# Optimization experiments

Measured on AMD Instinct MI355X. Metric: run time of the kernel, lower is better.

## Reference

```python
import jax, jax.numpy as jnp
import numpy as np

B, S, NX, NH = 4, 1024, 1024, 16
HD = NX // NH  # 64


def setup_inputs() -> dict:
    key = jax.random.key(0)
    k1, k2, k3 = jax.random.split(key, 3)
    return {
        "hidden_states": jax.random.normal(k1, (B, S, NX), dtype=jnp.float32),
        "c_attn_w": jax.random.normal(k2, (NX, 3 * NX), dtype=jnp.float32) * 0.02,
        "c_attn_b": jnp.zeros((3 * NX,), dtype=jnp.float32),
        "c_proj_w": jax.random.normal(k3, (NX, NX), dtype=jnp.float32) * 0.02,
        "c_proj_b": jnp.zeros((NX,), dtype=jnp.float32),
    }


def reference(hidden_states, c_attn_w, c_attn_b, c_proj_w, c_proj_b):
    # Conv1D fused QKV projection: x @ W + b, then split into q,k,v
    qkv = hidden_states @ c_attn_w + c_attn_b  # [B,S,3*NX]
    q, k, v = jnp.split(qkv, 3, axis=-1)
    # split heads -> [B, H, S, D]
    def heads(x):
        return x.reshape(B, S, NH, HD).transpose(0, 2, 1, 3)
    q, k, v = heads(q), heads(k), heads(v)
    # scores: q @ k^T / sqrt(D)  (scale=True; NOTE: no causal mask in this fork)
    w = jnp.einsum("bhqd,bhkd->bhqk", q, k) / jnp.sqrt(jnp.asarray(HD, q.dtype))
    w = jax.nn.softmax(w, axis=-1)
    a = jnp.einsum("bhqk,bhkd->bhqd", w, v)  # [B,H,S,D]
    # merge heads -> [B,S,NX]
    a = a.transpose(0, 2, 1, 3).reshape(B, S, NX)
    # output projection (dropout is identity in eval)
    return a @ c_proj_w + c_proj_b
```

## Files before the change

kernel.cpp:

```cpp
#include <hip/hip_runtime.h>
#include <hip/hip_fp16.h>
#include <cmath>

constexpr int Bb  = 4;
constexpr int Ss  = 1024;
constexpr int NXc = 1024;
constexpr int NHc = 16;
constexpr int HDc = 64;

typedef __bf16    bf16x8 __attribute__((ext_vector_type(8)));
typedef _Float16  f16x8  __attribute__((ext_vector_type(8)));
typedef float     f32x4  __attribute__((ext_vector_type(4)));
typedef unsigned short ushortT;
typedef ushortT ushort8v __attribute__((ext_vector_type(8)));

#define QSCALE 0.18033688011112042f

__device__ __forceinline__ ushortT f2h_bits(float x) {
  return __half_as_ushort(__float2half(x));
}

__device__ __forceinline__ void gll16(const void* g, void* l) {
  __builtin_amdgcn_global_load_lds(
      (const __attribute__((address_space(1))) unsigned int*)g,
      (__attribute__((address_space(3))) unsigned int*)l, 16, 0, 0);
}

__device__ __forceinline__ void drain_vmem() {
  asm volatile("s_waitcnt vmcnt(0)" ::: "memory");
  __builtin_amdgcn_sched_barrier(0);
}

__global__ __launch_bounds__(256) void prep_all(
    const float* __restrict__ hs, const float* __restrict__ aw,
    const float* __restrict__ pw,
    ushortT* __restrict__ hF, ushortT* __restrict__ awT,
    ushortT* __restrict__ pwT)
{
  const int bid = blockIdx.x;
  if (bid < 4096) {
    int i = (bid * 256 + threadIdx.x) * 4;
    float4 v = *reinterpret_cast<const float4*>(&hs[i]);
    *reinterpret_cast<ushort4*>(&hF[i]) =
        make_ushort4(f2h_bits(v.x), f2h_bits(v.y), f2h_bits(v.z), f2h_bits(v.w));
    return;
  }
  __shared__ float tile[32][33];
  const int tx = threadIdx.x & 31, ty = threadIdx.x >> 5;
  if (bid < 7168) {
    const int b2 = bid - 4096;
    const int n0 = (b2 % 96) * 32, k0 = (b2 / 96) * 32;
    #pragma unroll
    for (int i = 0; i < 4; ++i)
      tile[ty + i * 8][tx] = aw[(size_t)(k0 + ty + i * 8) * 3072 + n0 + tx];
    __syncthreads();
    #pragma unroll
    for (int i = 0; i < 4; ++i)
      awT[(size_t)(n0 + ty + i * 8) * 1024 + k0 + tx] = f2h_bits(tile[tx][ty + i * 8]);
  } else {
    const int b2 = bid - 7168;
    const int n0 = (b2 & 31) * 32, k0 = (b2 >> 5) * 32;
    #pragma unroll
    for (int i = 0; i < 4; ++i)
      tile[ty + i * 8][tx] = pw[(size_t)(k0 + ty + i * 8) * 1024 + n0 + tx];
    __syncthreads();
    #pragma unroll
    for (int i = 0; i < 4; ++i)
      pwT[(size_t)(n0 + ty + i * 8) * 1024 + k0 + tx] = f2h_bits(tile[tx][ty + i * 8]);
  }
}

__global__ __launch_bounds__(256) void gemm_f16_qkv(
    const ushortT* __restrict__ A16, const ushortT* __restrict__ B16,
    const float* __restrict__ bias,
    ushortT* __restrict__ Qb, ushortT* __restrict__ Kb,
    ushortT* __restrict__ Vt, int M, int N, int K)
{
  constexpr int BK = 64;
  __shared__ ushortT smem[32768];

  const int t    = threadIdx.x;
  const int lane = t & 63;
  const int w    = t >> 6;
  const int wr   = w >> 1, wc = w & 1;
  const int lin = blockIdx.y * 24 + blockIdx.x;
  const int swz = (lin & 7) * 96 + (lin >> 3);
  const int m0 = (swz / 24) * 128;
  const int n0 = (swz % 24) * 128;
  const int l15 = lane & 15;
  const int g   = lane >> 4;

  const int srow  = w * 32 + (lane >> 3);
  const int sslot = (lane & 7) ^ (lane >> 3);

  f32x4 acc[4][4];
  #pragma unroll
  for (int m = 0; m < 4; ++m)
    #pragma unroll
    for (int n = 0; n < 4; ++n)
      #pragma unroll
      for (int r = 0; r < 4; ++r) acc[m][n][r] = 0.f;

  const ushortT* pA = A16 + (size_t)(m0 + srow) * K + sslot * 8;
  const ushortT* pB = B16 + (size_t)(n0 + srow) * K + sslot * 8;

  auto STAGE = [&](ushortT* buf, int k0) {
    #pragma unroll
    for (int i = 0; i < 4; ++i) {
      const size_t gstep = (size_t)i * 8 * K + k0;
      const int    loff  = (w * 32 + i * 8) * BK;
      gll16(pA + gstep, &buf[loff]);
      gll16(pB + gstep, &buf[8192 + loff]);
    }
  };

  const int arow = wr * 64 + l15;
  const int bcol = wc * 64 + l15;

  auto COMPUTE = [&](const ushortT* buf) {
    const ushortT* sA = buf;
    const ushortT* sB = buf + 8192;
    #pragma unroll
    for (int c = 0; c < 2; ++c) {
      const int slot = c * 4 + g;
      f16x8 af[4], bf[4];
      #pragma unroll
      for (int m = 0; m < 4; ++m) {
        int r   = arow + m * 16;
        int off = r * BK + ((slot ^ (r & 7)) * 8);
        af[m] = *reinterpret_cast<const f16x8*>(&sA[off]);
      }
      #pragma unroll
      for (int n = 0; n < 4; ++n) {
        int r   = bcol + n * 16;
        int off = r * BK + ((slot ^ (r & 7)) * 8);
        bf[n] = *reinterpret_cast<const f16x8*>(&sB[off]);
      }
      #pragma unroll
      for (int m = 0; m < 4; ++m)
        #pragma unroll
        for (int n = 0; n < 4; ++n)
          acc[m][n] = __builtin_amdgcn_mfma_f32_16x16x32_f16(af[m], bf[n], acc[m][n], 0, 0, 0);
    }
  };

  const int nt = K / BK;
  STAGE(&smem[0], 0);
  drain_vmem();
  __syncthreads();
  for (int tt = 0; tt < nt; tt += 2) {
    if (tt + 1 < nt) STAGE(&smem[16384], (tt + 1) * BK);
    COMPUTE(&smem[0]);
    drain_vmem();
    __syncthreads();
    if (tt + 2 < nt) STAGE(&smem[0], (tt + 2) * BK);
    COMPUTE(&smem[16384]);
    drain_vmem();
    __syncthreads();
  }

  const int region = n0 >> 10;
  if (region < 2) {
    #pragma unroll
    for (int n = 0; n < 4; ++n) {
      int col_g = n0 + wc * 64 + n * 16 + l15;
      int colm  = col_g & 1023;
      float bv  = bias[col_g];
      #pragma unroll
      for (int m = 0; m < 4; ++m) {
        int row = m0 + wr * 64 + m * 16 + (g << 2);
        #pragma unroll
        for (int r = 0; r < 4; ++r) {
          float v = acc[m][n][r] + bv;
          if (region == 0)
            Qb[(size_t)(row + r) * 1024 + colm] = f2h_bits(v * QSCALE);
          else
            Kb[(size_t)(row + r) * 1024 + colm] = f2h_bits(v);
        }
      }
    }
  } else {
    ushortT* T = smem;
    #pragma unroll
    for (int n = 0; n < 4; ++n) {
      int cl   = wc * 64 + n * 16 + l15;
      float bv = bias[n0 + cl];
      #pragma unroll
      for (int m = 0; m < 4; ++m) {
        int rl = wr * 64 + m * 16 + (g << 2);
        #pragma unroll
        for (int r = 0; r < 4; ++r)
          T[cl * 136 + rl + r] = f2h_bits(acc[m][n][r] + bv);
      }
    }
    __syncthreads();
    const int c  = t >> 1;
    const int rh = (t & 1) * 64;
    const int nn = (n0 - 2048) + c;
    const int hh = nn >> 6, dd = nn & 63;
    const int bb = m0 >> 10;
    const int sl = (m0 & 1023) + rh;
    size_t vbase = ((size_t)((bb * 16 + hh) * 64 + dd)) * 1024 + sl;
    #pragma unroll
    for (int j = 0; j < 8; ++j) {
      ushort8v v = *reinterpret_cast<const ushort8v*>(&T[c * 136 + rh + j * 8]);
      *reinterpret_cast<ushort8v*>(&Vt[vbase + j * 8]) = v;
    }
  }
}

__global__ __launch_bounds__(256) void gemm_f16s(
    const ushortT* __restrict__ A16, const ushortT* __restrict__ B16,
    const float* __restrict__ bias, float* __restrict__ C,
    int M, int N, int K)
{
  constexpr int BK = 64;
  __shared__ ushortT smem[32768];

  const int t    = threadIdx.x;
  const int lane = t & 63;
  const int w    = t >> 6;
  const int wr   = w >> 1, wc = w & 1;
  const int lin = blockIdx.y * 8 + blockIdx.x;
  const int swz = (lin & 7) * 32 + (lin >> 3);
  const int m0 = (swz / 8) * 128;
  const int n0 = (swz % 8) * 128;
  const int l15 = lane & 15;
  const int g   = lane >> 4;

  const int srow  = w * 32 + (lane >> 3);
  const int sslot = (lane & 7) ^ (lane >> 3);

  f32x4 acc[4][4];
  #pragma unroll
  for (int m = 0; m < 4; ++m)
    #pragma unroll
    for (int n = 0; n < 4; ++n)
      #pragma unroll
      for (int r = 0; r < 4; ++r) acc[m][n][r] = 0.f;

  const ushortT* pA = A16 + (size_t)(m0 + srow) * K + sslot * 8;
  const ushortT* pB = B16 + (size_t)(n0 + srow) * K + sslot * 8;

  auto STAGE = [&](ushortT* buf, int k0) {
    #pragma unroll
    for (int i = 0; i < 4; ++i) {
      const size_t gstep = (size_t)i * 8 * K + k0;
      const int    loff  = (w * 32 + i * 8) * BK;
      gll16(pA + gstep, &buf[loff]);
      gll16(pB + gstep, &buf[8192 + loff]);
    }
  };

  const int arow = wr * 64 + l15;
  const int bcol = wc * 64 + l15;

  auto COMPUTE = [&](const ushortT* buf) {
    const ushortT* sA = buf;
    const ushortT* sB = buf + 8192;
    #pragma unroll
    for (int c = 0; c < 2; ++c) {
      const int slot = c * 4 + g;
      f16x8 af[4], bf[4];
      #pragma unroll
      for (int m = 0; m < 4; ++m) {
        int r   = arow + m * 16;
        int off = r * BK + ((slot ^ (r & 7)) * 8);
        af[m] = *reinterpret_cast<const f16x8*>(&sA[off]);
      }
      #pragma unroll
      for (int n = 0; n < 4; ++n) {
        int r   = bcol + n * 16;
        int off = r * BK + ((slot ^ (r & 7)) * 8);
        bf[n] = *reinterpret_cast<const f16x8*>(&sB[off]);
      }
      #pragma unroll
      for (int m = 0; m < 4; ++m)
        #pragma unroll
        for (int n = 0; n < 4; ++n)
          acc[m][n] = __builtin_amdgcn_mfma_f32_16x16x32_f16(af[m], bf[n], acc[m][n], 0, 0, 0);
    }
  };

  const int nt = K / BK;
  STAGE(&smem[0], 0);
  drain_vmem();
  __syncthreads();
  for (int tt = 0; tt < nt; tt += 2) {
    if (tt + 1 < nt) STAGE(&smem[16384], (tt + 1) * BK);
    COMPUTE(&smem[0]);
    drain_vmem();
    __syncthreads();
    if (tt + 2 < nt) STAGE(&smem[0], (tt + 2) * BK);
    COMPUTE(&smem[16384]);
    drain_vmem();
    __syncthreads();
  }

  #pragma unroll
  for (int n = 0; n < 4; ++n) {
    int col  = n0 + wc * 64 + n * 16 + l15;
    float bv = bias[col];
    #pragma unroll
    for (int m = 0; m < 4; ++m) {
      int row = m0 + wr * 64 + m * 16 + (g << 2);
      #pragma unroll
      for (int r = 0; r < 4; ++r)
        C[(size_t)(row + r) * N + col] = acc[m][n][r] + bv;
    }
  }
}

__global__ __launch_bounds__(256) void attn_mfma(
    const ushortT* __restrict__ Qb, const ushortT* __restrict__ Kb,
    const ushortT* __restrict__ Vt, ushortT* __restrict__ xF)
{
  __shared__ ushortT sK[64 * 64];
  __shared__ ushortT sV[64 * 64];
  __shared__ ushortT sP[64 * 64];

  const int t    = threadIdx.x;
  const int lane = t & 63;
  const int w    = t >> 6;
  const int bh = blockIdx.x, b = bh >> 4, h = bh & 15;
  const int q0 = blockIdx.y * 64;
  const int l15 = lane & 15;
  const int g   = lane >> 4;

  f16x8 qa[2];
  #pragma unroll
  for (int ks = 0; ks < 2; ++ks) {
    size_t addr = (size_t)(b * 1024 + q0 + w * 16 + l15) * 1024
                  + h * 64 + ks * 32 + g * 8;
    qa[ks] = *reinterpret_cast<const f16x8*>(&Qb[addr]);
  }

  f16x8 ones;
  #pragma unroll
  for (int j = 0; j < 8; ++j) ones[j] = (_Float16)1.0f;

  const int srow  = lane >> 3;
  const int sslot = (lane & 7) ^ srow;

  f32x4 O[4];
  f32x4 lO;
  #pragma unroll
  for (int r = 0; r < 4; ++r) lO[r] = 0.f;
  #pragma unroll
  for (int n = 0; n < 4; ++n)
    #pragma unroll
    for (int r = 0; r < 4; ++r) O[n][r] = 0.f;

  for (int kt = 0; kt < 16; ++kt) {
    const int k0 = kt * 64;
    #pragma unroll
    for (int i = 0; i < 2; ++i) {
      int r = w * 16 + i * 8 + srow;
      gll16(&Kb[(size_t)(b * 1024 + k0 + r) * 1024 + h * 64 + sslot * 8],
            &sK[(w * 16 + i * 8) * 64]);
      gll16(&Vt[((size_t)bh * 64 + r) * 1024 + k0 + sslot * 8],
            &sV[(w * 16 + i * 8) * 64]);
    }
    __syncthreads();

    f32x4 sc[4];
    #pragma unroll
    for (int n = 0; n < 4; ++n)
      #pragma unroll
      for (int r = 0; r < 4; ++r) sc[n][r] = 0.f;

    __builtin_amdgcn_s_setprio(1);
    #pragma unroll
    for (int ks = 0; ks < 2; ++ks) {
      f16x8 kb[4];
      #pragma unroll
      for (int n = 0; n < 4; ++n) {
        int row = n * 16 + l15;
        kb[n] = *reinterpret_cast<const f16x8*>(
            &sK[row * 64 + (((g + ks * 4) ^ (row & 7)) * 8)]);
      }
      #pragma unroll
      for (int n = 0; n < 4; ++n)
        sc[n] = __builtin_amdgcn_mfma_f32_16x16x32_f16(qa[ks], kb[n], sc[n], 0, 0, 0);
    }
    __builtin_amdgcn_s_setprio(0);

    #pragma unroll
    for (int n = 0; n < 4; ++n)
      #pragma unroll
      for (int r = 0; r < 4; ++r)
        sc[n][r] = exp2f(sc[n][r]);

    #pragma unroll
    for (int n = 0; n < 4; ++n)
      #pragma unroll
      for (int r = 0; r < 4; ++r) {
        int prow = w * 16 + g * 4 + r;
        int c    = n * 16 + l15;
        int off2 = prow * 64 + ((((c >> 3) ^ (prow & 7)) << 3) | (c & 7));
        sP[off2] = f2h_bits(sc[n][r]);
      }

    __builtin_amdgcn_s_setprio(1);
    #pragma unroll
    for (int ks = 0; ks < 2; ++ks) {
      f16x8 vb[4], pa;
      #pragma unroll
      for (int n = 0; n < 4; ++n) {
        int rd = n * 16 + l15;
        vb[n] = *reinterpret_cast<const f16x8*>(
            &sV[rd * 64 + (((g + ks * 4) ^ (rd & 7)) * 8)]);
      }
      {
        int pr = w * 16 + l15;
        pa = *reinterpret_cast<const f16x8*>(
            &sP[pr * 64 + (((g + ks * 4) ^ (pr & 7)) * 8)]);
      }
      #pragma unroll
      for (int n = 0; n < 4; ++n)
        O[n] = __builtin_amdgcn_mfma_f32_16x16x32_f16(pa, vb[n], O[n], 0, 0, 0);
      lO = __builtin_amdgcn_mfma_f32_16x16x32_f16(pa, ones, lO, 0, 0, 0);
    }
    __builtin_amdgcn_s_setprio(0);
    __syncthreads();
  }

  #pragma unroll
  for (int r = 0; r < 4; ++r) {
    float inv = 1.f / lO[r];
    #pragma unroll
    for (int n = 0; n < 4; ++n) {
      size_t off = (size_t)(b * 1024 + q0 + w * 16 + g * 4 + r) * 1024
                   + h * 64 + n * 16 + l15;
      xF[off] = f2h_bits(O[n][r] * inv);
    }
  }
}

extern "C" void kernel_launch(void* const* d_in, const int* in_sizes, int n_in,
                              void* d_out, int out_size, void* d_ws, size_t ws_size,
                              hipStream_t stream) {
  const float* hs = (const float*)d_in[0];
  const float* aw = (const float*)d_in[1];
  const float* ab = (const float*)d_in[2];
  const float* pw = (const float*)d_in[3];
  const float* pb = (const float*)d_in[4];
  float* out = (float*)d_out;

  char* ws = (char*)d_ws;
  const int M = Bb * Ss;

  ushortT* hF  = (ushortT*)(ws);
  ushortT* awT = (ushortT*)(ws + ( 8u << 20));
  ushortT* pwT = (ushortT*)(ws + (14u << 20));
  ushortT* Qb  = (ushortT*)(ws + (18u << 20));
  ushortT* Kb  = (ushortT*)(ws + (26u << 20));
  ushortT* Vt  = (ushortT*)(ws + (34u << 20));
  ushortT* xF  = (ushortT*)(ws + (42u << 20));

  dim3 blk(256);

  prep_all<<<8192, blk, 0, stream>>>(hs, aw, pw, hF, awT, pwT);
  gemm_f16_qkv<<<dim3(24, 32), blk, 0, stream>>>(
      hF, awT, ab, Qb, Kb, Vt, M, 3 * NXc, NXc);
  attn_mfma<<<dim3(Bb * NHc, Ss / 64), blk, 0, stream>>>(Qb, Kb, Vt, xF);
  gemm_f16s<<<dim3(8, 32), blk, 0, stream>>>(
      xF, pwT, pb, out, M, NXc, NXc);
}
```

Before: 100.3 us.

## Split attention KV range across two blocks and combine partials in new kernel

Result: slower. 105.0 us (+4.7%).

```diff
diff --git a/kernel.cpp b/kernel.cpp
--- a/kernel.cpp
+++ b/kernel.cpp
@@ -18,6 +18,9 @@
 
 __device__ __forceinline__ ushortT f2h_bits(float x) {
   return __half_as_ushort(__float2half(x));
+}
+__device__ __forceinline__ float h2f(ushortT h) {
+  return __half2float(__ushort_as_half(h));
 }
 
 __device__ __forceinline__ void gll16(const void* g, void* l) {
@@ -313,7 +316,8 @@
 
 __global__ __launch_bounds__(256) void attn_mfma(
     const ushortT* __restrict__ Qb, const ushortT* __restrict__ Kb,
-    const ushortT* __restrict__ Vt, ushortT* __restrict__ xF)
+    const ushortT* __restrict__ Vt,
+    ushortT* __restrict__ Op, float* __restrict__ lP)
 {
   __shared__ ushortT sK[64 * 64];
   __shared__ ushortT sV[64 * 64];
@@ -324,6 +328,7 @@
   const int w    = t >> 6;
   const int bh = blockIdx.x, b = bh >> 4, h = bh & 15;
   const int q0 = blockIdx.y * 64;
+  const int half = blockIdx.z;
   const int l15 = lane & 15;
   const int g   = lane >> 4;
 
@@ -351,7 +356,7 @@
     #pragma unroll
     for (int r = 0; r < 4; ++r) O[n][r] = 0.f;
 
-  for (int kt = 0; kt < 16; ++kt) {
+  for (int kt = half * 8; kt < half * 8 + 8; ++kt) {
     const int k0 = kt * 64;
     #pragma unroll
     for (int i = 0; i < 2; ++i) {
@@ -369,7 +374,6 @@
       #pragma unroll
       for (int r = 0; r < 4; ++r) sc[n][r] = 0.f;
 
-    __builtin_amdgcn_s_setprio(1);
     #pragma unroll
     for (int ks = 0; ks < 2; ++ks) {
       f16x8 kb[4];
@@ -383,7 +387,6 @@
       for (int n = 0; n < 4; ++n)
         sc[n] = __builtin_amdgcn_mfma_f32_16x16x32_f16(qa[ks], kb[n], sc[n], 0, 0, 0);
     }
-    __builtin_amdgcn_s_setprio(0);
 
     #pragma unroll
     for (int n = 0; n < 4; ++n)
@@ -401,7 +404,6 @@
         sP[off2] = f2h_bits(sc[n][r]);
       }
 
-    __builtin_amdgcn_s_setprio(1);
     #pragma unroll
     for (int ks = 0; ks < 2; ++ks) {
       f16x8 vb[4], pa;
@@ -421,20 +423,42 @@
         O[n] = __builtin_amdgcn_mfma_f32_16x16x32_f16(pa, vb[n], O[n], 0, 0, 0);
       lO = __builtin_amdgcn_mfma_f32_16x16x32_f16(pa, ones, lO, 0, 0, 0);
     }
-    __builtin_amdgcn_s_setprio(0);
-    __syncthreads();
-  }
-
+    __syncthreads();
+  }
+
+  const size_t obase = (size_t)half * (4096ull * 1024ull);
   #pragma unroll
   for (int r = 0; r < 4; ++r) {
-    float inv = 1.f / lO[r];
+    int qrow = q0 + w * 16 + g * 4 + r;
+    if (l15 == 0)
+      lP[half * 65536 + (b * 16 + h) * 1024 + qrow] = lO[r];
     #pragma unroll
     for (int n = 0; n < 4; ++n) {
-      size_t off = (size_t)(b * 1024 + q0 + w * 16 + g * 4 + r) * 1024
-                   + h * 64 + n * 16 + l15;
-      xF[off] = f2h_bits(O[n][r] * inv);
-    }
-  }
+      size_t off = obase + (size_t)(b * 1024 + qrow) * 1024 + h * 64 + n * 16 + l15;
+      Op[off] = f2h_bits(O[n][r]);
+    }
+  }
+}
+
+__global__ __launch_bounds__(256) void combine_kernel(
+    const ushortT* __restrict__ Op, const float* __restrict__ lP,
+    ushortT* __restrict__ xF)
+{
+  int i = (blockIdx.x * 256 + threadIdx.x) * 8;
+  int row = i >> 10;
+  int col = i & 1023;
+  int b = row >> 10;
+  int q = row & 1023;
+  int h = col >> 6;
+  int lidx = (b * 16 + h) * 1024 + q;
+  float inv = 1.f / (lP[lidx] + lP[65536 + lidx]);
+  ushort8v o1 = *reinterpret_cast<const ushort8v*>(&Op[i]);
+  ushort8v o2 = *reinterpret_cast<const ushort8v*>(&Op[4194304 + i]);
+  ushort8v o;
+  #pragma unroll
+  for (int j = 0; j < 8; ++j)
+    o[j] = f2h_bits((h2f(o1[j]) + h2f(o2[j])) * inv);
+  *reinterpret_cast<ushort8v*>(&xF[i]) = o;
 }
 
 extern "C" void kernel_launch(void* const* d_in, const int* in_sizes, int n_in,
@@ -457,13 +481,16 @@
   ushortT* Kb  = (ushortT*)(ws + (26u << 20));
   ushortT* Vt  = (ushortT*)(ws + (34u << 20));
   ushortT* xF  = (ushortT*)(ws + (42u << 20));
+  ushortT* Op  = (ushortT*)(ws + (50u << 20));
+  float*   lP  = (float*)  (ws + (66u << 20));
 
   dim3 blk(256);
 
   prep_all<<<8192, blk, 0, stream>>>(hs, aw, pw, hF, awT, pwT);
   gemm_f16_qkv<<<dim3(24, 32), blk, 0, stream>>>(
       hF, awT, ab, Qb, Kb, Vt, M, 3 * NXc, NXc);
-  attn_mfma<<<dim3(Bb * NHc, Ss / 64), blk, 0, stream>>>(Qb, Kb, Vt, xF);
+  attn_mfma<<<dim3(Bb * NHc, Ss / 64, 2), blk, 0, stream>>>(Qb, Kb, Vt, Op, lP);
+  combine_kernel<<<2048, blk, 0, stream>>>(Op, lP, xF);
   gemm_f16s<<<dim3(8, 32), blk, 0, stream>>>(
       xF, pwT, pb, out, M, NXc, NXc);
 }
```
